# Kernel tuning notes

Measured on AMD Instinct MI355X. Metric: run time of the kernel, lower is better.

## Reference

```python
import jax, jax.numpy as jnp
import numpy as np

B, C_IN, T = 64, 512, 16
C_OUT, K, E = 512, 3, 16


def setup_inputs() -> dict:
    key = jax.random.key(0)
    k1, k2, k3, k4, k5 = jax.random.split(key, 5)
    x = jax.random.normal(k1, (B, C_IN, T), dtype=jnp.float32)
    rf_w = jax.random.normal(k2, (E, C_IN), dtype=jnp.float32) * 0.02   # 1x1 conv kernel (E, c_in)
    rf_b = jax.random.normal(k3, (E,), dtype=jnp.float32) * 0.02
    weight = jax.random.normal(k4, (E, C_OUT, C_IN, K), dtype=jnp.float32) * 0.02  # expert bank
    bias = jax.random.normal(k5, (E, C_OUT), dtype=jnp.float32) * 0.02
    return {"x": x, "rf_w": rf_w, "rf_b": rf_b, "weight": weight, "bias": bias}


def reference(x, rf_w, rf_b, weight, bias):
    b, c, t = x.shape
    e, c_out, c_in, k = weight.shape
    # global avg pool over T, then 1x1 conv == linear: (B, E)
    pooled = x.mean(axis=2)
    rf = pooled @ rf_w.T + rf_b
    # per-sample synthesized conv kernels (B, c_out, c_in, k) and biases (B, c_out)
    w = jnp.einsum('be,eoik->boik', rf, weight)
    bb = rf @ bias
    # grouped conv1d (groups=b) == per-sample conv; im2col via k shifted views (k=3, fixed)
    p = k // 2
    x_pad = jnp.pad(x, ((0, 0), (0, 0), (p, p)))
    win = jnp.stack([x_pad[:, :, j:j + t] for j in range(k)], axis=2)  # (B, c_in, k, T)
    out = jnp.einsum('boik,bikt->bot', w, win) + bb[:, :, None] + 1.0
    return out
```

## Files before the change

### kernel.cpp

```cpp
#include <hip/hip_runtime.h>


__global__ __launch_bounds__(256) void k1_transpose_pool(const float* __restrict__ x,
                                                         float* __restrict__ pooled,
                                                         float* __restrict__ xt) {
  int g = blockIdx.x * 256 + threadIdx.x;
  int c = g >> 6;
  int b = g & 63;
  const float4* xb = (const float4*)(x + ((size_t)b * 512 + c) * 16);
  float4 v0 = xb[0], v1 = xb[1], v2 = xb[2], v3 = xb[3];
  float s = v0.x + v0.y + v0.z + v0.w + v1.x + v1.y + v1.z + v1.w +
            v2.x + v2.y + v2.z + v2.w + v3.x + v3.y + v3.z + v3.w;
  pooled[c * 64 + b] = s * 0.0625f;
  float4* row = (float4*)(xt + ((size_t)c * 64 + b) * 20);
  row[0] = make_float4(0.f, v0.x, v0.y, v0.z);
  row[1] = make_float4(v0.w, v1.x, v1.y, v1.z);
  row[2] = make_float4(v1.w, v2.x, v2.y, v2.z);
  row[3] = make_float4(v2.w, v3.x, v3.y, v3.z);
  row[4] = make_float4(v3.w, 0.f, 0.f, 0.f);
}

__global__ __launch_bounds__(256) void k1b_rf(const float* __restrict__ pooled,
                                              const float* __restrict__ rf_w,
                                              const float* __restrict__ rf_b,
                                              float* __restrict__ rf) {
  __shared__ __align__(16) float ps[16 * 520];
  __shared__ __align__(16) float wsm[16 * 520];
  int tid = threadIdx.x, bg = blockIdx.x;
#pragma unroll
  for (int j = 0; j < 8; ++j) {
    int g = tid + j * 256;
    int e = g >> 7, q = g & 127;
    *(float4*)&wsm[e * 520 + q * 4] = *(const float4*)&rf_w[e * 512 + q * 4];
  }
#pragma unroll
  for (int j = 0; j < 8; ++j) {
    int g = tid + j * 256;
    int c = g >> 2, q = g & 3;
    float4 v = *(const float4*)&pooled[c * 64 + bg * 16 + q * 4];
    ps[(q * 4 + 0) * 520 + c] = v.x;
    ps[(q * 4 + 1) * 520 + c] = v.y;
    ps[(q * 4 + 2) * 520 + c] = v.z;
    ps[(q * 4 + 3) * 520 + c] = v.w;
  }
  __syncthreads();
  int bl = tid >> 4, e = tid & 15;
  const float4* pr = (const float4*)&ps[bl * 520];
  const float4* wr = (const float4*)&wsm[e * 520];
  float s0 = 0, s1 = 0, s2 = 0, s3 = 0;
#pragma unroll 8
  for (int c4 = 0; c4 < 128; ++c4) {
    float4 p = pr[c4];
    float4 w = wr[c4];
    s0 = fmaf(p.x, w.x, s0);
    s1 = fmaf(p.y, w.y, s1);
    s2 = fmaf(p.z, w.z, s2);
    s3 = fmaf(p.w, w.w, s3);
  }
  rf[(bg * 16 + bl) * 16 + e] = s0 + s1 + s2 + s3 + rf_b[e];
}

__global__ __launch_bounds__(256) void k2_main(const float* __restrict__ weight,
                                               const float* __restrict__ xt,
                                               const float* __restrict__ rf,
                                               float* __restrict__ part) {
  __shared__ __align__(16) float xs[8 * 64 * 20];
  const int tid = threadIdx.x;
  const int b = tid & 63;
  const int og = __builtin_amdgcn_readfirstlane(tid >> 6);
  const int o0 = blockIdx.x * 8 + og * 2;
  const int ic = blockIdx.y;
  float rfv[16];
#pragma unroll
  for (int e = 0; e < 16; ++e) rfv[e] = rf[b * 16 + e];
  float acc0[16], acc1[16];
#pragma unroll
  for (int t = 0; t < 16; ++t) { acc0[t] = 0.f; acc1[t] = 0.f; }
  const float* wb = weight + (size_t)o0 * 1536;
#pragma unroll 1
  for (int sub = 0; sub < 8; ++sub) {
    const int i0 = ic * 64 + sub * 8;
    __syncthreads();
    const float4* src = (const float4*)(xt + (size_t)i0 * 1280);
    float4* dst = (float4*)xs;
#pragma unroll
    for (int j = 0; j < 10; ++j) dst[tid + j * 256] = src[tid + j * 256];
    __syncthreads();
#pragma unroll
    for (int ii = 0; ii < 8; ++ii) {
      const int i = i0 + ii;
      const float* wp = wb + i * 3;
      float w00 = 0, w01 = 0, w02 = 0, w10 = 0, w11 = 0, w12 = 0;
#pragma unroll
      for (int e = 0; e < 16; ++e) {
        const float* we = wp + e * 786432;
        float r = rfv[e];
        w00 = fmaf(r, we[0], w00);
        w01 = fmaf(r, we[1], w01);
        w02 = fmaf(r, we[2], w02);
        w10 = fmaf(r, we[1536], w10);
        w11 = fmaf(r, we[1537], w11);
        w12 = fmaf(r, we[1538], w12);
      }
      const float* xr = &xs[(ii * 64 + b) * 20];
      float xv[18];
      *(float4*)&xv[0] = *(const float4*)&xr[0];
      *(float4*)&xv[4] = *(const float4*)&xr[4];
      *(float4*)&xv[8] = *(const float4*)&xr[8];
      *(float4*)&xv[12] = *(const float4*)&xr[12];
      *(float2*)&xv[16] = *(const float2*)&xr[16];
#pragma unroll
      for (int t = 0; t < 16; ++t) {
        float a0 = acc0[t], a1 = acc1[t];
        a0 = fmaf(w00, xv[t], a0);
        a0 = fmaf(w01, xv[t + 1], a0);
        a0 = fmaf(w02, xv[t + 2], a0);
        a1 = fmaf(w10, xv[t], a1);
        a1 = fmaf(w11, xv[t + 1], a1);
        a1 = fmaf(w12, xv[t + 2], a1);
        acc0[t] = a0;
        acc1[t] = a1;
      }
    }
  }
  float4* p4 = (float4*)(part + (((size_t)ic * 64 + b) * 512 + o0) * 16);
#pragma unroll
  for (int t4 = 0; t4 < 4; ++t4)
    p4[t4] = make_float4(acc0[t4 * 4], acc0[t4 * 4 + 1], acc0[t4 * 4 + 2], acc0[t4 * 4 + 3]);
#pragma unroll
  for (int t4 = 0; t4 < 4; ++t4)
    p4[4 + t4] = make_float4(acc1[t4 * 4], acc1[t4 * 4 + 1], acc1[t4 * 4 + 2], acc1[t4 * 4 + 3]);
}

__global__ __launch_bounds__(256) void k3_reduce(const float* __restrict__ part,
                                                 const float* __restrict__ rf,
                                                 const float* __restrict__ bias,
                                                 float* __restrict__ out) {
  int g = blockIdx.x * 256 + threadIdx.x;
  int b = g >> 11;
  int o = (g >> 2) & 511;
  float4 s = make_float4(1.f, 1.f, 1.f, 1.f);
#pragma unroll
  for (int ic = 0; ic < 8; ++ic) {
    float4 p = ((const float4*)part)[ic * 131072 + g];
    s.x += p.x;
    s.y += p.y;
    s.z += p.z;
    s.w += p.w;
  }
  int bu = __builtin_amdgcn_readfirstlane(b);
  float bb = 0.f;
#pragma unroll
  for (int e = 0; e < 16; ++e) bb = fmaf(rf[bu * 16 + e], bias[e * 512 + o], bb);
  s.x += bb;
  s.y += bb;
  s.z += bb;
  s.w += bb;
  ((float4*)out)[g] = s;
}

extern "C" void kernel_launch(void* const* d_in, const int* in_sizes, int n_in,
                              void* d_out, int out_size, void* d_ws, size_t ws_size,
                              hipStream_t stream) {
  const float* x = (const float*)d_in[0];
  const float* rf_w = (const float*)d_in[1];
  const float* rf_b = (const float*)d_in[2];
  const float* weight = (const float*)d_in[3];
  const float* bias = (const float*)d_in[4];
  float* out = (float*)d_out;
  float* ws = (float*)d_ws;

  float* rf = ws;
  float* pooled = ws + 1024;
  float* xt = ws + 33792;
  float* part = ws + 689152;

  k1_transpose_pool<<<128, 256, 0, stream>>>(x, pooled, xt);
  k1b_rf<<<4, 256, 0, stream>>>(pooled, rf_w, rf_b, rf);
  k2_main<<<dim3(64, 8), 256, 0, stream>>>(weight, xt, rf, part);
  k3_reduce<<<512, 256, 0, stream>>>(part, rf, bias, out);
}
```

Baseline: 234.0 us.

## Transpose xt to time-major layout and register-prefetch input tiles in main kernel

The transposed input buffer now stores time in the outer dimension with batch innermost, so shared-memory reads across the 64 batch lanes are contiguous and avoid bank conflicts. The main kernel gives each wave one output channel instead of two, doubling the grid. It loads the next 4-channel input tile into registers while computing the current one, and reads weights as float4 vectors covering 4 input channels at a time. This lowers per-thread register pressure and overlaps global loads with compute. In exchange, k1's writes become strided scalar stores, and each weight element is now loaded by twice as many blocks because reuse across output pairs is gone.

```diff
diff --git a/kernel.cpp b/kernel.cpp
--- a/kernel.cpp
+++ b/kernel.cpp
@@ -12,12 +12,15 @@
   float s = v0.x + v0.y + v0.z + v0.w + v1.x + v1.y + v1.z + v1.w +
             v2.x + v2.y + v2.z + v2.w + v3.x + v3.y + v3.z + v3.w;
   pooled[c * 64 + b] = s * 0.0625f;
-  float4* row = (float4*)(xt + ((size_t)c * 64 + b) * 20);
-  row[0] = make_float4(0.f, v0.x, v0.y, v0.z);
-  row[1] = make_float4(v0.w, v1.x, v1.y, v1.z);
-  row[2] = make_float4(v1.w, v2.x, v2.y, v2.z);
-  row[3] = make_float4(v2.w, v3.x, v3.y, v3.z);
-  row[4] = make_float4(v3.w, 0.f, 0.f, 0.f);
+  float* col = xt + (size_t)c * 1280 + b;
+  float xv[16] = {v0.x, v0.y, v0.z, v0.w, v1.x, v1.y, v1.z, v1.w,
+                  v2.x, v2.y, v2.z, v2.w, v3.x, v3.y, v3.z, v3.w};
+  col[0] = 0.f;
+#pragma unroll
+  for (int t = 0; t < 16; ++t) col[(t + 1) * 64] = xv[t];
+  col[17 * 64] = 0.f;
+  col[18 * 64] = 0.f;
+  col[19 * 64] = 0.f;
 }
 
 __global__ __launch_bounds__(256) void k1b_rf(const float* __restrict__ pooled,
@@ -64,72 +67,82 @@
                                                const float* __restrict__ xt,
                                                const float* __restrict__ rf,
                                                float* __restrict__ part) {
-  __shared__ __align__(16) float xs[8 * 64 * 20];
+  __shared__ __align__(16) float xs[4 * 20 * 64];
   const int tid = threadIdx.x;
   const int b = tid & 63;
-  const int og = __builtin_amdgcn_readfirstlane(tid >> 6);
-  const int o0 = blockIdx.x * 8 + og * 2;
+  const int wv = __builtin_amdgcn_readfirstlane(tid >> 6);
+  const int o = blockIdx.x * 4 + wv;
   const int ic = blockIdx.y;
+
   float rfv[16];
 #pragma unroll
   for (int e = 0; e < 16; ++e) rfv[e] = rf[b * 16 + e];
-  float acc0[16], acc1[16];
+  float acc[16];
 #pragma unroll
-  for (int t = 0; t < 16; ++t) { acc0[t] = 0.f; acc1[t] = 0.f; }
-  const float* wb = weight + (size_t)o0 * 1536;
+  for (int t = 0; t < 16; ++t) acc[t] = 0.f;
+
+  const float* wbase = weight + (size_t)o * 1536;
+  const float4* xt4 = (const float4*)xt;
+
+  float4 xr[5];
+  {
+    int i0 = ic * 64;
+#pragma unroll
+    for (int j = 0; j < 5; ++j) xr[j] = xt4[i0 * 320 + tid + j * 256];
+  }
+
 #pragma unroll 1
-  for (int sub = 0; sub < 8; ++sub) {
-    const int i0 = ic * 64 + sub * 8;
-    __syncthreads();
-    const float4* src = (const float4*)(xt + (size_t)i0 * 1280);
-    float4* dst = (float4*)xs;
-#pragma unroll
-    for (int j = 0; j < 10; ++j) dst[tid + j * 256] = src[tid + j * 256];
+  for (int sub = 0; sub < 16; ++sub) {
+    const int i0 = ic * 64 + sub * 4;
     __syncthreads();
 #pragma unroll
-    for (int ii = 0; ii < 8; ++ii) {
-      const int i = i0 + ii;
-      const float* wp = wb + i * 3;
-      float w00 = 0, w01 = 0, w02 = 0, w10 = 0, w11 = 0, w12 = 0;
+    for (int j = 0; j < 5; ++j) ((float4*)xs)[tid + j * 256] = xr[j];
+    __syncthreads();
+    if (sub + 1 < 16) {
+      int i1 = i0 + 4;
 #pragma unroll
-      for (int e = 0; e < 16; ++e) {
-        const float* we = wp + e * 786432;
-        float r = rfv[e];
-        w00 = fmaf(r, we[0], w00);
-        w01 = fmaf(r, we[1], w01);
-        w02 = fmaf(r, we[2], w02);
-        w10 = fmaf(r, we[1536], w10);
-        w11 = fmaf(r, we[1537], w11);
-        w12 = fmaf(r, we[1538], w12);
-      }
-      const float* xr = &xs[(ii * 64 + b) * 20];
-      float xv[18];
-      *(float4*)&xv[0] = *(const float4*)&xr[0];
-      *(float4*)&xv[4] = *(const float4*)&xr[4];
-      *(float4*)&xv[8] = *(const float4*)&xr[8];
-      *(float4*)&xv[12] = *(const float4*)&xr[12];
-      *(float2*)&xv[16] = *(const float2*)&xr[16];
+      for (int j = 0; j < 5; ++j) xr[j] = xt4[i1 * 320 + tid + j * 256];
+    }
+    float wsyn[4][3];
 #pragma unroll
-      for (int t = 0; t < 16; ++t) {
-        float a0 = acc0[t], a1 = acc1[t];
-        a0 = fmaf(w00, xv[t], a0);
-        a0 = fmaf(w01, xv[t + 1], a0);
-        a0 = fmaf(w02, xv[t + 2], a0);
-        a1 = fmaf(w10, xv[t], a1);
-        a1 = fmaf(w11, xv[t + 1], a1);
-        a1 = fmaf(w12, xv[t + 2], a1);
-        acc0[t] = a0;
-        acc1[t] = a1;
+    for (int ii = 0; ii < 4; ++ii) {
+      wsyn[ii][0] = 0.f; wsyn[ii][1] = 0.f; wsyn[ii][2] = 0.f;
+    }
+#pragma unroll
+    for (int e = 0; e < 16; ++e) {
+      const float4* wp4 = (const float4*)(wbase + (size_t)e * 786432 + i0 * 3);
+      float4 q0 = wp4[0], q1 = wp4[1], q2 = wp4[2];
+      float r = rfv[e];
+      wsyn[0][0] = fmaf(r, q0.x, wsyn[0][0]);
+      wsyn[0][1] = fmaf(r, q0.y, wsyn[0][1]);
+      wsyn[0][2] = fmaf(r, q0.z, wsyn[0][2]);
+      wsyn[1][0] = fmaf(r, q0.w, wsyn[1][0]);
+      wsyn[1][1] = fmaf(r, q1.x, wsyn[1][1]);
+      wsyn[1][2] = fmaf(r, q1.y, wsyn[1][2]);
+      wsyn[2][0] = fmaf(r, q1.z, wsyn[2][0]);
+      wsyn[2][1] = fmaf(r, q1.w, wsyn[2][1]);
+      wsyn[2][2] = fmaf(r, q2.x, wsyn[2][2]);
+      wsyn[3][0] = fmaf(r, q2.y, wsyn[3][0]);
+      wsyn[3][1] = fmaf(r, q2.z, wsyn[3][1]);
+      wsyn[3][2] = fmaf(r, q2.w, wsyn[3][2]);
+    }
+#pragma unroll
+    for (int ii = 0; ii < 4; ++ii) {
+      const float w0 = wsyn[ii][0], w1 = wsyn[ii][1], w2 = wsyn[ii][2];
+      const float* xcol = xs + ii * 1280 + b;
+#pragma unroll
+      for (int tp = 0; tp < 18; ++tp) {
+        float xv = xcol[tp * 64];
+        if (tp < 16) acc[tp] = fmaf(w0, xv, acc[tp]);
+        if (tp >= 1 && tp <= 16) acc[tp - 1] = fmaf(w1, xv, acc[tp - 1]);
+        if (tp >= 2) acc[tp - 2] = fmaf(w2, xv, acc[tp - 2]);
       }
     }
   }
-  float4* p4 = (float4*)(part + (((size_t)ic * 64 + b) * 512 + o0) * 16);
+  float4* p4 = (float4*)(part + (((size_t)ic * 64 + b) * 512 + o) * 16);
 #pragma unroll
   for (int t4 = 0; t4 < 4; ++t4)
-    p4[t4] = make_float4(acc0[t4 * 4], acc0[t4 * 4 + 1], acc0[t4 * 4 + 2], acc0[t4 * 4 + 3]);
-#pragma unroll
-  for (int t4 = 0; t4 < 4; ++t4)
-    p4[4 + t4] = make_float4(acc1[t4 * 4], acc1[t4 * 4 + 1], acc1[t4 * 4 + 2], acc1[t4 * 4 + 3]);
+    p4[t4] = make_float4(acc[t4 * 4], acc[t4 * 4 + 1], acc[t4 * 4 + 2], acc[t4 * 4 + 3]);
 }
 
 __global__ __launch_bounds__(256) void k3_reduce(const float* __restrict__ part,
@@ -177,6 +190,6 @@
 
   k1_transpose_pool<<<128, 256, 0, stream>>>(x, pooled, xt);
   k1b_rf<<<4, 256, 0, stream>>>(pooled, rf_w, rf_b, rf);
-  k2_main<<<dim3(64, 8), 256, 0, stream>>>(weight, xt, rf, part);
+  k2_main<<<dim3(128, 8), 256, 0, stream>>>(weight, xt, rf, part);
   k3_reduce<<<512, 256, 0, stream>>>(part, rf, bias, out);
 }
```

After: 368.9 us. 57.6% more time.
